# Kernel tuning notes

Measured on AMD Instinct MI355X. Metric: run time of the kernel, lower is better.

Reference implementation:

```python
import jax, jax.numpy as jnp
import numpy as np

C_OUT = 16
C_IN = 16
L0 = 64        # layer_sizes[0]
H = 128        # hidden width
D_IN = C_IN * L0  # 1024, flattened per-point input dim


def _uniform(key, shape, fan_in):
    bound = 1.0 / np.sqrt(fan_in)
    return jax.random.uniform(key, shape, jnp.float32, -bound, bound)


def setup_inputs() -> dict:
    key = jax.random.key(0)
    ks = jax.random.split(key, 7)
    x = jax.random.normal(ks[0], (65536, C_IN, L0), jnp.float32)
    # Stacked per-output-channel MLP weights (torch Linear transposed: [in, out])
    W1 = _uniform(ks[1], (C_OUT, D_IN, H), D_IN)
    b1 = _uniform(ks[2], (C_OUT, H), D_IN)
    W2 = _uniform(ks[3], (C_OUT, H, H), H)
    b2 = _uniform(ks[4], (C_OUT, H, H)[:2], H)
    W3 = _uniform(ks[5], (C_OUT, H, 1), H)
    b3 = _uniform(ks[6], (C_OUT, 1), H)
    return {"x": x, "W1": W1, "b1": b1, "W2": W2, "b2": b2, "W3": W3, "b3": b3}


def reference(x, W1, b1, W2, b2, W3, b3):
    # x: [N, C_in, L0] -> flatten per point to [N, D_IN]
    N = x.shape[0]
    xf = x.reshape(N, -1)
    # Batched per-output-channel GEMMs (replaces Python loop over channels_out)
    h = jax.nn.relu(jnp.einsum('nd,cdh->cnh', xf, W1) + b1[:, None, :])   # [C, N, H]
    h = jax.nn.relu(jnp.einsum('cnh,chk->cnk', h, W2) + b2[:, None, :])   # [C, N, H]
    out = jnp.einsum('cnh,cho->cno', h, W3) + b3[:, None, :]              # [C, N, 1]
    # squeeze(-1) then permute channel axis to the end: [N, C_out]
    return out[..., 0].T
```

## Files before the change

### kernel.cpp

```cpp
#include <hip/hip_runtime.h>
#include <cstdint>

typedef unsigned short u16;
typedef __attribute__((ext_vector_type(4))) float f32x4;
typedef __attribute__((ext_vector_type(8))) __bf16 bf16x8;
typedef __attribute__((ext_vector_type(8))) u16 u16x8;
typedef __attribute__((ext_vector_type(4))) u16 u16x4;

#define C_OUT 16
#define D_IN 1024
#define HDIM 128
#define NPTS 65536
#define BN 128
#define BK 64

__device__ __forceinline__ u16 f2bf(float f){
  uint32_t u = __builtin_bit_cast(uint32_t, f);
  u += 0x7FFFu + ((u >> 16) & 1u);
  return (u16)(u >> 16);
}

__device__ __forceinline__ void gload_lds16(const void* g, void* l){
  __builtin_amdgcn_global_load_lds((const __attribute__((address_space(1))) void*)g,
                                   (__attribute__((address_space(3))) void*)l, 16, 0, 0);
}

__global__ __launch_bounds__(256) void transpose_cvt(const float* __restrict__ src,
                                                     u16* __restrict__ dst, int R, int C){
  __shared__ float tile[32][33];
  int ch = blockIdx.z;
  int r0 = blockIdx.y * 32, c0 = blockIdx.x * 32;
  const float* s = src + (size_t)ch * R * C;
  u16* d = dst + (size_t)ch * R * C;
  int tx = threadIdx.x, ty = threadIdx.y;
  for (int i = ty; i < 32; i += 8) tile[i][tx] = s[(size_t)(r0 + i) * C + c0 + tx];
  __syncthreads();
  for (int i = ty; i < 32; i += 8) d[(size_t)(c0 + i) * R + r0 + tx] = f2bf(tile[tx][i]);
}

__global__ __launch_bounds__(256) void cvt_x_kernel(const float4* __restrict__ src,
                                                    u16x4* __restrict__ dst, int n4){
  int stride = gridDim.x * 256;
  for (int i = blockIdx.x * 256 + threadIdx.x; i < n4; i += stride){
    float4 v = src[i];
    u16x4 o = { f2bf(v.x), f2bf(v.y), f2bf(v.z), f2bf(v.w) };
    dst[i] = o;
  }
}

template<bool XBF16>
__global__ __launch_bounds__(256, 3) void mlp_fused(const void* __restrict__ xsrc,
    const u16* __restrict__ W1T, const u16* __restrict__ W2T,
    const float* __restrict__ b1, const float* __restrict__ b2,
    const float* __restrict__ W3, const float* __restrict__ b3,
    float* __restrict__ out){
  __shared__ __align__(16) u16 smem[2 * BN * BK];
  __shared__ float outb[BN];
  u16* As = smem;
  u16* Bs = smem + BN * BK;

  const int t = threadIdx.x;
  const int wave = t >> 6, lane = t & 63;
  const int q = lane >> 4, s = lane & 15;
  const int wr = (wave >> 1) * 64, wc = (wave & 1) * 64;
  const int c = blockIdx.x & 15;
  const int n0 = (blockIdx.x >> 4) * BN;

  const u16* w1c = W1T + (size_t)c * HDIM * D_IN;

  f32x4 acc[4][4];
#pragma unroll
  for (int i = 0; i < 4; i++)
#pragma unroll
    for (int j = 0; j < 4; j++) acc[i][j] = (f32x4){0.f, 0.f, 0.f, 0.f};

  for (int kt = 0; kt < D_IN / BK; kt++){
#pragma unroll
    for (int ii = 0; ii < 4; ii++){
      int hbase = wave * 32 + ii * 8;
      int h = hbase + (lane >> 3);
      int k = kt * BK + (((lane & 7) ^ (h & 7)) * 8);
      gload_lds16(w1c + (size_t)h * D_IN + k, &Bs[hbase * BK]);
    }
    if (XBF16){
      const u16* xb = (const u16*)xsrc;
#pragma unroll
      for (int ii = 0; ii < 4; ii++){
        int rbase = wave * 32 + ii * 8;
        int row = rbase + (lane >> 3);
        int k = kt * BK + (((lane & 7) ^ (row & 7)) * 8);
        gload_lds16(xb + (size_t)(n0 + row) * D_IN + k, &As[rbase * BK]);
      }
    } else {
      const float* xf = (const float*)xsrc;
#pragma unroll
      for (int rr = 0; rr < 4; rr++){
        int row = rr * 32 + (t >> 3);
        const float* srcp = xf + (size_t)(n0 + row) * D_IN + kt * BK + (t & 7) * 8;
        float4 v0 = *(const float4*)srcp;
        float4 v1 = *(const float4*)(srcp + 4);
        u16x8 p = { f2bf(v0.x), f2bf(v0.y), f2bf(v0.z), f2bf(v0.w),
                    f2bf(v1.x), f2bf(v1.y), f2bf(v1.z), f2bf(v1.w) };
        int sc = (t & 7) ^ (row & 7);
        *(u16x8*)&As[row * BK + sc * 8] = p;
      }
    }
    __syncthreads();
#pragma unroll
    for (int ks = 0; ks < 2; ks++){
      bf16x8 a[4], b[4];
#pragma unroll
      for (int i = 0; i < 4; i++){
        int m = wr + i * 16 + s;
        int ch = ks * 4 + q;
        a[i] = __builtin_bit_cast(bf16x8, *(const u16x8*)&As[m * BK + ((ch ^ (m & 7)) * 8)]);
      }
#pragma unroll
      for (int j = 0; j < 4; j++){
        int hh = wc + j * 16 + s;
        int ch = ks * 4 + q;
        b[j] = __builtin_bit_cast(bf16x8, *(const u16x8*)&Bs[hh * BK + ((ch ^ (hh & 7)) * 8)]);
      }
#pragma unroll
      for (int i = 0; i < 4; i++)
#pragma unroll
        for (int j = 0; j < 4; j++)
          acc[i][j] = __builtin_amdgcn_mfma_f32_16x16x32_bf16(a[i], b[j], acc[i][j], 0, 0, 0);
    }
    __syncthreads();
  }

  float b1v[4];
#pragma unroll
  for (int j = 0; j < 4; j++) b1v[j] = b1[c * HDIM + wc + j * 16 + s];
  u16* h1s = smem;
#pragma unroll
  for (int i = 0; i < 4; i++)
#pragma unroll
    for (int j = 0; j < 4; j++)
#pragma unroll
      for (int r = 0; r < 4; r++){
        float v = fmaxf(acc[i][j][r] + b1v[j], 0.f);
        int m = wr + i * 16 + q * 4 + r;
        int h = wc + j * 16 + s;
        h1s[m * HDIM + (((h >> 3) ^ (m & 7)) * 8) + (h & 7)] = f2bf(v);
      }
  __syncthreads();

  const u16* w2c = W2T + (size_t)c * HDIM * HDIM;
  f32x4 acc2[4][4];
#pragma unroll
  for (int i = 0; i < 4; i++)
#pragma unroll
    for (int j = 0; j < 4; j++) acc2[i][j] = (f32x4){0.f, 0.f, 0.f, 0.f};
#pragma unroll
  for (int ks = 0; ks < 4; ks++){
    bf16x8 a[4], b[4];
#pragma unroll
    for (int i = 0; i < 4; i++){
      int m = wr + i * 16 + s;
      int ch = ks * 4 + q;
      a[i] = __builtin_bit_cast(bf16x8, *(const u16x8*)&h1s[m * HDIM + ((ch ^ (m & 7)) * 8)]);
    }
#pragma unroll
    for (int j = 0; j < 4; j++){
      int col = wc + j * 16 + s;
      b[j] = __builtin_bit_cast(bf16x8, *(const u16x8*)(w2c + (size_t)col * HDIM + ks * 32 + q * 8));
    }
#pragma unroll
    for (int i = 0; i < 4; i++)
#pragma unroll
      for (int j = 0; j < 4; j++)
        acc2[i][j] = __builtin_amdgcn_mfma_f32_16x16x32_bf16(a[i], b[j], acc2[i][j], 0, 0, 0);
  }

  float b2v[4], w3v[4];
#pragma unroll
  for (int j = 0; j < 4; j++){
    b2v[j] = b2[c * HDIM + wc + j * 16 + s];
    w3v[j] = W3[c * HDIM + wc + j * 16 + s];
  }
  float part[4][4];
#pragma unroll
  for (int i = 0; i < 4; i++)
#pragma unroll
    for (int r = 0; r < 4; r++) part[i][r] = 0.f;
#pragma unroll
  for (int i = 0; i < 4; i++)
#pragma unroll
    for (int j = 0; j < 4; j++)
#pragma unroll
      for (int r = 0; r < 4; r++){
        float hv = fmaxf(acc2[i][j][r] + b2v[j], 0.f);
        part[i][r] = fmaf(hv, w3v[j], part[i][r]);
      }
#pragma unroll
  for (int mask = 1; mask <= 8; mask <<= 1)
#pragma unroll
    for (int i = 0; i < 4; i++)
#pragma unroll
      for (int r = 0; r < 4; r++) part[i][r] += __shfl_xor(part[i][r], mask, 64);

  if (s == 0 && wc == 0){
#pragma unroll
    for (int i = 0; i < 4; i++)
#pragma unroll
      for (int r = 0; r < 4; r++) outb[wr + i * 16 + q * 4 + r] = part[i][r];
  }
  __syncthreads();
  if (s == 0 && wc == 64){
#pragma unroll
    for (int i = 0; i < 4; i++)
#pragma unroll
      for (int r = 0; r < 4; r++) outb[wr + i * 16 + q * 4 + r] += part[i][r];
  }
  __syncthreads();
  if (t < BN) out[(size_t)(n0 + t) * C_OUT + c] = outb[t] + b3[c];
}

__global__ __launch_bounds__(256) void mlp_naive(const float* __restrict__ x,
    const float* __restrict__ W1, const float* __restrict__ b1,
    const float* __restrict__ W2, const float* __restrict__ b2,
    const float* __restrict__ W3, const float* __restrict__ b3,
    float* __restrict__ out){
  __shared__ float xs[16 * D_IN];
  __shared__ float h1[16 * HDIM];
  __shared__ float h2[16 * HDIM];
  int c = blockIdx.x & 15;
  int n0 = (blockIdx.x >> 4) * 16;
  int t = threadIdx.x;
  for (int i = t; i < 16 * D_IN; i += 256) xs[i] = x[(size_t)n0 * D_IN + i];
  __syncthreads();
  int h = t & 127, ng = t >> 7;
  const float* w1c = W1 + (size_t)c * D_IN * HDIM;
  float a1[8];
#pragma unroll
  for (int nn = 0; nn < 8; nn++) a1[nn] = 0.f;
  for (int d = 0; d < D_IN; d++){
    float w = w1c[(size_t)d * HDIM + h];
#pragma unroll
    for (int nn = 0; nn < 8; nn++) a1[nn] = fmaf(xs[(ng * 8 + nn) * D_IN + d], w, a1[nn]);
  }
  float bb = b1[c * HDIM + h];
#pragma unroll
  for (int nn = 0; nn < 8; nn++) h1[(ng * 8 + nn) * HDIM + h] = fmaxf(a1[nn] + bb, 0.f);
  __syncthreads();
  const float* w2c = W2 + (size_t)c * HDIM * HDIM;
  float a2[8];
#pragma unroll
  for (int nn = 0; nn < 8; nn++) a2[nn] = 0.f;
  for (int k = 0; k < HDIM; k++){
    float w = w2c[(size_t)k * HDIM + h];
#pragma unroll
    for (int nn = 0; nn < 8; nn++) a2[nn] = fmaf(h1[(ng * 8 + nn) * HDIM + k], w, a2[nn]);
  }
  bb = b2[c * HDIM + h];
#pragma unroll
  for (int nn = 0; nn < 8; nn++) h2[(ng * 8 + nn) * HDIM + h] = fmaxf(a2[nn] + bb, 0.f);
  __syncthreads();
  if (t < 16){
    float ssum = 0.f;
    for (int hh = 0; hh < HDIM; hh++) ssum = fmaf(h2[t * HDIM + hh], W3[c * HDIM + hh], ssum);
    out[(size_t)(n0 + t) * C_OUT + c] = ssum + b3[c];
  }
}

extern "C" void kernel_launch(void* const* d_in, const int* in_sizes, int n_in,
                              void* d_out, int out_size, void* d_ws, size_t ws_size,
                              hipStream_t stream){
  const float* x  = (const float*)d_in[0];
  const float* W1 = (const float*)d_in[1];
  const float* b1 = (const float*)d_in[2];
  const float* W2 = (const float*)d_in[3];
  const float* b2 = (const float*)d_in[4];
  const float* W3 = (const float*)d_in[5];
  const float* b3 = (const float*)d_in[6];
  float* out = (float*)d_out;

  const size_t W1T_elems = (size_t)C_OUT * HDIM * D_IN;
  const size_t W2T_elems = (size_t)C_OUT * HDIM * HDIM;
  const size_t ws_w_bytes = (W1T_elems + W2T_elems) * 2;
  const size_t xb_bytes   = (size_t)NPTS * D_IN * 2;

  if (ws_size < ws_w_bytes){
    mlp_naive<<<(NPTS / 16) * C_OUT, 256, 0, stream>>>(x, W1, b1, W2, b2, W3, b3, out);
    return;
  }

  u16* W1T = (u16*)d_ws;
  u16* W2T = W1T + W1T_elems;
  transpose_cvt<<<dim3(HDIM / 32, D_IN / 32, C_OUT), dim3(32, 8), 0, stream>>>(W1, W1T, D_IN, HDIM);
  transpose_cvt<<<dim3(HDIM / 32, HDIM / 32, C_OUT), dim3(32, 8), 0, stream>>>(W2, W2T, HDIM, HDIM);

  const int grid = (NPTS / BN) * C_OUT;
  if (ws_size >= ws_w_bytes + xb_bytes){
    u16* xb = W2T + W2T_elems;
    cvt_x_kernel<<<8192, 256, 0, stream>>>((const float4*)x, (u16x4*)xb, NPTS * D_IN / 4);
    mlp_fused<true><<<grid, 256, 0, stream>>>(xb, W1T, W2T, b1, b2, W3, b3, out);
  } else {
    mlp_fused<false><<<grid, 256, 0, stream>>>(x, W1T, W2T, b1, b2, W3, b3, out);
  }
}
```

Measured before the change: 690.3 us.

## Drop x pre-conversion pass and prefetch fp32 x into registers in fused MLP

Removes the separate kernel that converted x to bf16 in workspace and makes the fused MLP always read fp32 x, converting in-kernel. The next k-tile of x is prefetched into registers while the current tile is being computed, to hide global latency. This eliminates a full read/write pass over x. The trade-off is more register pressure, redundant conversion work across the 16 channel blocks, and doubled cached x traffic per block.

```diff
diff --git a/kernel.cpp b/kernel.cpp
--- a/kernel.cpp
+++ b/kernel.cpp
@@ -5,7 +5,6 @@
 typedef __attribute__((ext_vector_type(4))) float f32x4;
 typedef __attribute__((ext_vector_type(8))) __bf16 bf16x8;
 typedef __attribute__((ext_vector_type(8))) u16 u16x8;
-typedef __attribute__((ext_vector_type(4))) u16 u16x4;
 
 #define C_OUT 16
 #define D_IN 1024
@@ -38,18 +37,7 @@
   for (int i = ty; i < 32; i += 8) d[(size_t)(c0 + i) * R + r0 + tx] = f2bf(tile[tx][i]);
 }
 
-__global__ __launch_bounds__(256) void cvt_x_kernel(const float4* __restrict__ src,
-                                                    u16x4* __restrict__ dst, int n4){
-  int stride = gridDim.x * 256;
-  for (int i = blockIdx.x * 256 + threadIdx.x; i < n4; i += stride){
-    float4 v = src[i];
-    u16x4 o = { f2bf(v.x), f2bf(v.y), f2bf(v.z), f2bf(v.w) };
-    dst[i] = o;
-  }
-}
-
-template<bool XBF16>
-__global__ __launch_bounds__(256, 3) void mlp_fused(const void* __restrict__ xsrc,
+__global__ __launch_bounds__(256, 3) void mlp_fused(const float* __restrict__ xf,
     const u16* __restrict__ W1T, const u16* __restrict__ W2T,
     const float* __restrict__ b1, const float* __restrict__ b2,
     const float* __restrict__ W3, const float* __restrict__ b3,
@@ -74,6 +62,17 @@
 #pragma unroll
     for (int j = 0; j < 4; j++) acc[i][j] = (f32x4){0.f, 0.f, 0.f, 0.f};
 
+  const int arow = t >> 3;
+  const int alc  = t & 7;
+  float4 pv0[4], pv1[4];
+#pragma unroll
+  for (int rr = 0; rr < 4; rr++){
+    int row = rr * 32 + arow;
+    const float* p = xf + (size_t)(n0 + row) * D_IN + alc * 8;
+    pv0[rr] = *(const float4*)p;
+    pv1[rr] = *(const float4*)(p + 4);
+  }
+
   for (int kt = 0; kt < D_IN / BK; kt++){
 #pragma unroll
     for (int ii = 0; ii < 4; ii++){
@@ -82,30 +81,24 @@
       int k = kt * BK + (((lane & 7) ^ (h & 7)) * 8);
       gload_lds16(w1c + (size_t)h * D_IN + k, &Bs[hbase * BK]);
     }
-    if (XBF16){
-      const u16* xb = (const u16*)xsrc;
-#pragma unroll
-      for (int ii = 0; ii < 4; ii++){
-        int rbase = wave * 32 + ii * 8;
-        int row = rbase + (lane >> 3);
-        int k = kt * BK + (((lane & 7) ^ (row & 7)) * 8);
-        gload_lds16(xb + (size_t)(n0 + row) * D_IN + k, &As[rbase * BK]);
-      }
-    } else {
-      const float* xf = (const float*)xsrc;
+#pragma unroll
+    for (int rr = 0; rr < 4; rr++){
+      int row = rr * 32 + arow;
+      u16x8 pk = { f2bf(pv0[rr].x), f2bf(pv0[rr].y), f2bf(pv0[rr].z), f2bf(pv0[rr].w),
+                   f2bf(pv1[rr].x), f2bf(pv1[rr].y), f2bf(pv1[rr].z), f2bf(pv1[rr].w) };
+      int sc = alc ^ (row & 7);
+      *(u16x8*)&As[row * BK + sc * 8] = pk;
+    }
+    __syncthreads();
+    if (kt + 1 < D_IN / BK){
 #pragma unroll
       for (int rr = 0; rr < 4; rr++){
-        int row = rr * 32 + (t >> 3);
-        const float* srcp = xf + (size_t)(n0 + row) * D_IN + kt * BK + (t & 7) * 8;
-        float4 v0 = *(const float4*)srcp;
-        float4 v1 = *(const float4*)(srcp + 4);
-        u16x8 p = { f2bf(v0.x), f2bf(v0.y), f2bf(v0.z), f2bf(v0.w),
-                    f2bf(v1.x), f2bf(v1.y), f2bf(v1.z), f2bf(v1.w) };
-        int sc = (t & 7) ^ (row & 7);
-        *(u16x8*)&As[row * BK + sc * 8] = p;
-      }
-    }
-    __syncthreads();
+        int row = rr * 32 + arow;
+        const float* p = xf + (size_t)(n0 + row) * D_IN + (kt + 1) * BK + alc * 8;
+        pv0[rr] = *(const float4*)p;
+        pv1[rr] = *(const float4*)(p + 4);
+      }
+    }
 #pragma unroll
     for (int ks = 0; ks < 2; ks++){
       bf16x8 a[4], b[4];
@@ -280,7 +273,6 @@
   const size_t W1T_elems = (size_t)C_OUT * HDIM * D_IN;
   const size_t W2T_elems = (size_t)C_OUT * HDIM * HDIM;
   const size_t ws_w_bytes = (W1T_elems + W2T_elems) * 2;
-  const size_t xb_bytes   = (size_t)NPTS * D_IN * 2;
 
   if (ws_size < ws_w_bytes){
     mlp_naive<<<(NPTS / 16) * C_OUT, 256, 0, stream>>>(x, W1, b1, W2, b2, W3, b3, out);
@@ -293,11 +285,5 @@
   transpose_cvt<<<dim3(HDIM / 32, HDIM / 32, C_OUT), dim3(32, 8), 0, stream>>>(W2, W2T, HDIM, HDIM);
 
   const int grid = (NPTS / BN) * C_OUT;
-  if (ws_size >= ws_w_bytes + xb_bytes){
-    u16* xb = W2T + W2T_elems;
-    cvt_x_kernel<<<8192, 256, 0, stream>>>((const float4*)x, (u16x4*)xb, NPTS * D_IN / 4);
-    mlp_fused<true><<<grid, 256, 0, stream>>>(xb, W1T, W2T, b1, b2, W3, b3, out);
-  } else {
-    mlp_fused<false><<<grid, 256, 0, stream>>>(x, W1T, W2T, b1, b2, W3, b3, out);
-  }
-}
+  mlp_fused<<<grid, 256, 0, stream>>>(x, W1T, W2T, b1, b2, W3, b3, out);
+}
```

New measurement: 744.1 us. 7.8% more time.
